# Performance work log

Hardware: AMD Instinct MI355X
Metric: run time of the kernel (lower is better)

Reference implementation:

```python
import jax, jax.numpy as jnp
import numpy as np


def setup_inputs() -> dict:
    key = jax.random.key(0)
    k1, k2 = jax.random.split(key)
    B, N, M, K = 8, 4096, 4096, 64
    input1 = jax.random.normal(k1, (B, N, K), dtype=jnp.float32)
    input2 = jax.random.normal(k2, (B, M, K), dtype=jnp.float32)
    return {"input1": input1, "input2": input2}


def reference(input1, input2):
    # Pairwise L2 distances via the ||x||^2 + ||y||^2 - 2<x,y> identity,
    # avoiding the O(B*N*M*K) broadcast-subtraction intermediate.
    x2 = jnp.sum(input1 * input1, axis=-1)                 # [B, N]
    y2 = jnp.sum(input2 * input2, axis=-1)                 # [B, M]
    xy = jnp.einsum('bnk,bmk->bnm', input1, input2)        # [B, N, M]
    sq = x2[:, :, None] + y2[:, None, :] - 2.0 * xy
    D = jnp.sqrt(jnp.maximum(sq, 0.0))                     # [B, N, M]
    dist0 = jnp.mean(jnp.min(D, axis=1), axis=1)           # min over N, mean over M
    dist1 = jnp.mean(jnp.min(D, axis=2), axis=1)           # min over M, mean over N
    loss = jnp.mean(dist0 + dist1)
    return loss
```

## Files before the change

### kernel.cpp

```cpp
#include <hip/hip_runtime.h>

#define BATCH 8
#define NPTS  4096
#define KD    64
#define MQ    4
#define WALK  8
#define FINF  3.0e38f

typedef float f32x4 __attribute__((ext_vector_type(4)));
typedef float f32x2 __attribute__((ext_vector_type(2)));
typedef short s16x8 __attribute__((ext_vector_type(8)));

__device__ __forceinline__ unsigned int f2bf(float f) {
  unsigned int u = __float_as_uint(f);
  u += 0x7FFFu + ((u >> 16) & 1u);
  return u >> 16;
}

__device__ __forceinline__ void stage16(const void* g, void* l) {
  __builtin_amdgcn_global_load_lds((const __attribute__((address_space(1))) void*)g,
                                   (__attribute__((address_space(3))) void*)l, 16, 0, 0);
}

__global__ __launch_bounds__(256)
void prep_kernel(const float* __restrict__ X, const float* __restrict__ Y,
                 unsigned int* __restrict__ Xbf, unsigned int* __restrict__ Ybf,
                 float* __restrict__ x2, float* __restrict__ y2,
                 unsigned int* __restrict__ counter) {
  int gid = blockIdx.x * 256 + threadIdx.x;
  if (gid == 0) *counter = 0;
  int row = gid >> 5;
  int ki  = gid & 31;
  bool isX = row < BATCH * NPTS;
  int r2 = row & (BATCH * NPTS - 1);
  const float* src = isX ? X : Y;
  f32x2 v = *(const f32x2*)(src + (size_t)r2 * KD + ki * 2);
  float s = v[0] * v[0] + v[1] * v[1];
  #pragma unroll
  for (int m = 16; m >= 1; m >>= 1) s += __shfl_xor(s, m, 64);
  unsigned int packed = (f2bf(v[1]) << 16) | f2bf(v[0]);
  (isX ? Xbf : Ybf)[r2 * 32 + ki] = packed;
  if (ki == 0) (isX ? x2 : y2)[r2] = s;
}

__global__ __launch_bounds__(256, 2)
void chamfer_main(const unsigned short* __restrict__ Xbf,
                  const unsigned short* __restrict__ Ybf,
                  const float* __restrict__ x2g, const float* __restrict__ y2g,
                  float* __restrict__ rowpart,
                  float* __restrict__ colpart) {
  __shared__ __align__(16) unsigned short Xs[128 * 64];
  __shared__ __align__(16) unsigned short Ys[2][128 * 64];
  __shared__ float l_cred[2 * 2 * 128];

  const int mq = blockIdx.x, ntile = blockIdx.y, b = blockIdx.z;
  const int n0 = ntile * 128;
  const int mbase = mq * (WALK * 128);
  const int t = threadIdx.x, w = t >> 6, lane = t & 63, c = lane & 15, q = lane >> 4;
  const int wr = (w >> 1) * 64, wc = (w & 1) * 64, rg = w >> 1;

  const int l8 = lane >> 3;
  const int lane_off = l8 * 128 + (((lane & 7) ^ l8) << 4);

  const char* Xg  = (const char*)(Xbf + (size_t)(b * NPTS + n0) * KD);
  const char* Yg0 = (const char*)(Ybf + (size_t)(b * NPTS + mbase) * KD);

  #pragma unroll
  for (int k = 0; k < 4; ++k) {
    int blockoff = (k * 32 + w * 8) * 128;
    int ldsoff   = (k * 256 + w * 64) * 16;
    stage16(Xg  + blockoff + lane_off, (char*)Xs    + ldsoff);
    stage16(Yg0 + blockoff + lane_off, (char*)Ys[0] + ldsoff);
  }

  const float* x2b = x2g + b * NPTS + n0;
  f32x4 x2r[4];
  #pragma unroll
  for (int i = 0; i < 4; ++i) x2r[i] = *(const f32x4*)(x2b + wr + i * 16 + q * 4);

  __syncthreads();

  const int cx = c & 7;
  s16x8 xf[4][2];
  #pragma unroll
  for (int i = 0; i < 4; ++i)
    #pragma unroll
    for (int ks = 0; ks < 2; ++ks)
      xf[i][ks] = *(const s16x8*)&Xs[(wr + i * 16 + c) * 64 + ((((ks << 2) + q) ^ cx) << 3)];

  float rm[4][4];
  #pragma unroll
  for (int i = 0; i < 4; ++i)
    #pragma unroll
    for (int r = 0; r < 4; ++r) rm[i][r] = FINF;

  const float* y2b = y2g + b * NPTS + mbase;
  float* colrow = colpart + (size_t)(ntile * 8 + b) * NPTS + mbase;
  const f32x4 zacc = {0.f, 0.f, 0.f, 0.f};

  #pragma unroll 2
  for (int tt = 0; tt < WALK; ++tt) {
    const unsigned short* cur = Ys[tt & 1];

    float y2c[4];
    #pragma unroll
    for (int j = 0; j < 4; ++j) y2c[j] = y2b[tt * 128 + wc + j * 16 + c];

    if (tt < WALK - 1) {
      const char* Ygt = Yg0 + (size_t)(tt + 1) * 128 * 128;
      unsigned short* nb = Ys[(tt + 1) & 1];
      #pragma unroll
      for (int k = 0; k < 4; ++k)
        stage16(Ygt + (k * 32 + w * 8) * 128 + lane_off,
                (char*)nb + (k * 256 + w * 64) * 16);
    }

    if (tt > 0 && t < 128) {
      int pt = tt - 1, pb = pt & 1;
      float v = fminf(l_cred[(pb * 2 + 0) * 128 + t], l_cred[(pb * 2 + 1) * 128 + t]);
      colrow[pt * 128 + t] = v + y2b[pt * 128 + t];
    }

    float cmj[4];
    #pragma unroll
    for (int j = 0; j < 4; ++j) {
      const unsigned short* yrow = &cur[(wc + j * 16 + c) * 64];
      s16x8 yf0 = *(const s16x8*)&yrow[(q ^ cx) << 3];
      s16x8 yf1 = *(const s16x8*)&yrow[((4 + q) ^ cx) << 3];
      f32x4 acc[4];
      #pragma unroll
      for (int i = 0; i < 4; ++i) {
        f32x4 a0 = __builtin_amdgcn_mfma_f32_16x16x32_bf16(xf[i][0], yf0, zacc, 0, 0, 0);
        acc[i] = __builtin_amdgcn_mfma_f32_16x16x32_bf16(xf[i][1], yf1, a0, 0, 0, 0);
      }
      float cm = FINF;
      #pragma unroll
      for (int i = 0; i < 4; ++i)
        #pragma unroll
        for (int r = 0; r < 4; ++r) {
          float v = acc[i][r];
          rm[i][r] = fminf(rm[i][r], fmaf(-2.f, v, y2c[j]));
          cm = fminf(cm, fmaf(-2.f, v, x2r[i][r]));
        }
      cm = fminf(cm, __shfl_xor(cm, 16, 64));
      cm = fminf(cm, __shfl_xor(cm, 32, 64));
      cmj[j] = cm;
    }
    float cmq = (q == 0) ? cmj[0] : (q == 1) ? cmj[1] : (q == 2) ? cmj[2] : cmj[3];
    l_cred[((tt & 1) * 2 + rg) * 128 + wc + q * 16 + c] = cmq;

    __syncthreads();
  }

  #pragma unroll
  for (int msk = 1; msk <= 8; msk <<= 1)
    #pragma unroll
    for (int i = 0; i < 4; ++i)
      #pragma unroll
      for (int r = 0; r < 4; ++r)
        rm[i][r] = fminf(rm[i][r], __shfl_xor(rm[i][r], msk, 64));
  float* l_redf = (float*)Xs;
  if (c == 0) {
    #pragma unroll
    for (int i = 0; i < 4; ++i) {
      f32x4 v = {rm[i][0], rm[i][1], rm[i][2], rm[i][3]};
      *(f32x4*)&l_redf[w * 64 + i * 16 + q * 4] = v;
    }
  }
  __syncthreads();

  if (t < 128) {
    {
      int pt = WALK - 1, pb = pt & 1;
      float v = fminf(l_cred[(pb * 2 + 0) * 128 + t], l_cred[(pb * 2 + 1) * 128 + t]);
      colrow[pt * 128 + t] = v + y2b[pt * 128 + t];
    }
    int g = t >> 6, lr = t & 63;
    float v = fminf(l_redf[(g * 2) * 64 + lr], l_redf[(g * 2 + 1) * 64 + lr]);
    rowpart[mq * (BATCH * NPTS) + b * NPTS + n0 + t] = v + x2b[t];
  }
}

__global__ __launch_bounds__(256)
void reduce_kernel(const float* __restrict__ rowpart, const float* __restrict__ colpart,
                   float* __restrict__ partials, unsigned int* __restrict__ counter,
                   float* __restrict__ out) {
  int i = blockIdx.x * 256 + threadIdx.x;
  const int TOT = BATCH * NPTS;
  float rv = FINF;
  #pragma unroll
  for (int s = 0; s < MQ; ++s) rv = fminf(rv, rowpart[s * TOT + i]);
  float s0 = sqrtf(fmaxf(rv, 0.f));
  float cv = FINF;
  #pragma unroll
  for (int nt = 0; nt < 32; ++nt) cv = fminf(cv, colpart[nt * TOT + i]);
  s0 += sqrtf(fmaxf(cv, 0.f));
  #pragma unroll
  for (int m = 32; m >= 1; m >>= 1) s0 += __shfl_xor(s0, m, 64);
  __shared__ float wsum[4];
  if ((threadIdx.x & 63) == 0) wsum[threadIdx.x >> 6] = s0;
  __syncthreads();

  if (threadIdx.x < 64) {
    unsigned int ticket = 0;
    if (threadIdx.x == 0) {
      float bsum = wsum[0] + wsum[1] + wsum[2] + wsum[3];
      atomicExch(&partials[blockIdx.x], bsum);
      __threadfence();
      ticket = atomicAdd(counter, 1);
    }
    ticket = __shfl(ticket, 0, 64);
    if (ticket == 127) {
      float v = atomicAdd(&partials[threadIdx.x], 0.0f) +
                atomicAdd(&partials[threadIdx.x + 64], 0.0f);
      #pragma unroll
      for (int m = 32; m >= 1; m >>= 1) v += __shfl_xor(v, m, 64);
      if (threadIdx.x == 0) out[0] = v * (1.0f / (float)TOT);
    }
  }
}

extern "C" void kernel_launch(void* const* d_in, const int* in_sizes, int n_in,
                              void* d_out, int out_size, void* d_ws, size_t ws_size,
                              hipStream_t stream) {
  const float* X = (const float*)d_in[0];
  const float* Y = (const float*)d_in[1];
  float* out = (float*)d_out;

  char* ws = (char*)d_ws;
  unsigned int* Xbf = (unsigned int*)ws;
  unsigned int* Ybf = (unsigned int*)(ws + (4u << 20));
  float* x2 = (float*)(ws + (8u << 20));
  float* y2 = (float*)(ws + (8u << 20) + (128u << 10));
  float* rowpart = (float*)(ws + (8u << 20) + (256u << 10));
  float* colpart = (float*)(ws + (9u << 20) + (256u << 10));
  float* partials = (float*)(ws + (13u << 20) + (256u << 10));
  unsigned int* counter = (unsigned int*)(partials + 128);

  prep_kernel<<<dim3(2 * BATCH * NPTS * 32 / 256), dim3(256), 0, stream>>>(
      X, Y, Xbf, Ybf, x2, y2, counter);

  chamfer_main<<<dim3(MQ, 32, 8), dim3(256), 0, stream>>>(
      (const unsigned short*)Xbf, (const unsigned short*)Ybf, x2, y2, rowpart, colpart);

  reduce_kernel<<<dim3(BATCH * NPTS / 256), dim3(256), 0, stream>>>(
      rowpart, colpart, partials, counter, out);
}
```

Before: 106.8 us.

## Load X fragments directly from global and cut one cross-lane shuffle per column

Removes the shared-memory staging buffer for the X tile. Each wave now loads its bf16 X fragments straight from global memory into registers, which frees LDS (possibly improving occupancy) and drops one LDS round trip. The column-min reduction now does a single xor-16 shuffle instead of two and writes four partial slots per column into a padded LDS buffer, with the final min over the four slots done by the reducing threads. The trade-off is uncoalesced 16-byte global loads for X and extra LDS reads in the column reduction.

```diff
diff --git a/kernel.cpp b/kernel.cpp
--- a/kernel.cpp
+++ b/kernel.cpp
@@ -49,9 +49,9 @@
                   const float* __restrict__ x2g, const float* __restrict__ y2g,
                   float* __restrict__ rowpart,
                   float* __restrict__ colpart) {
-  __shared__ __align__(16) unsigned short Xs[128 * 64];
   __shared__ __align__(16) unsigned short Ys[2][128 * 64];
-  __shared__ float l_cred[2 * 2 * 128];
+  __shared__ float l_credq[2 * 4 * 132];
+  __shared__ float l_redf[256];
 
   const int mq = blockIdx.x, ntile = blockIdx.y, b = blockIdx.z;
   const int n0 = ntile * 128;
@@ -62,16 +62,20 @@
   const int l8 = lane >> 3;
   const int lane_off = l8 * 128 + (((lane & 7) ^ l8) << 4);
 
-  const char* Xg  = (const char*)(Xbf + (size_t)(b * NPTS + n0) * KD);
+  const unsigned short* Xrow = Xbf + (size_t)(b * NPTS + n0) * KD;
   const char* Yg0 = (const char*)(Ybf + (size_t)(b * NPTS + mbase) * KD);
 
   #pragma unroll
-  for (int k = 0; k < 4; ++k) {
-    int blockoff = (k * 32 + w * 8) * 128;
-    int ldsoff   = (k * 256 + w * 64) * 16;
-    stage16(Xg  + blockoff + lane_off, (char*)Xs    + ldsoff);
-    stage16(Yg0 + blockoff + lane_off, (char*)Ys[0] + ldsoff);
-  }
+  for (int k = 0; k < 4; ++k)
+    stage16(Yg0 + (k * 32 + w * 8) * 128 + lane_off,
+            (char*)Ys[0] + (k * 256 + w * 64) * 16);
+
+  s16x8 xf[4][2];
+  #pragma unroll
+  for (int i = 0; i < 4; ++i)
+    #pragma unroll
+    for (int ks = 0; ks < 2; ++ks)
+      xf[i][ks] = *(const s16x8*)&Xrow[(size_t)(wr + i * 16 + c) * KD + (ks * 4 + q) * 8];
 
   const float* x2b = x2g + b * NPTS + n0;
   f32x4 x2r[4];
@@ -80,20 +84,13 @@
 
   __syncthreads();
 
+  float rm[4][4];
+  #pragma unroll
+  for (int i = 0; i < 4; ++i)
+    #pragma unroll
+    for (int r = 0; r < 4; ++r) rm[i][r] = FINF;
+
   const int cx = c & 7;
-  s16x8 xf[4][2];
-  #pragma unroll
-  for (int i = 0; i < 4; ++i)
-    #pragma unroll
-    for (int ks = 0; ks < 2; ++ks)
-      xf[i][ks] = *(const s16x8*)&Xs[(wr + i * 16 + c) * 64 + ((((ks << 2) + q) ^ cx) << 3)];
-
-  float rm[4][4];
-  #pragma unroll
-  for (int i = 0; i < 4; ++i)
-    #pragma unroll
-    for (int r = 0; r < 4; ++r) rm[i][r] = FINF;
-
   const float* y2b = y2g + b * NPTS + mbase;
   float* colrow = colpart + (size_t)(ntile * 8 + b) * NPTS + mbase;
   const f32x4 zacc = {0.f, 0.f, 0.f, 0.f};
@@ -117,7 +114,8 @@
 
     if (tt > 0 && t < 128) {
       int pt = tt - 1, pb = pt & 1;
-      float v = fminf(l_cred[(pb * 2 + 0) * 128 + t], l_cred[(pb * 2 + 1) * 128 + t]);
+      float v = fminf(fminf(l_credq[(pb * 4 + 0) * 132 + t], l_credq[(pb * 4 + 1) * 132 + t]),
+                      fminf(l_credq[(pb * 4 + 2) * 132 + t], l_credq[(pb * 4 + 3) * 132 + t]));
       colrow[pt * 128 + t] = v + y2b[pt * 128 + t];
     }
 
@@ -143,11 +141,17 @@
           cm = fminf(cm, fmaf(-2.f, v, x2r[i][r]));
         }
       cm = fminf(cm, __shfl_xor(cm, 16, 64));
-      cm = fminf(cm, __shfl_xor(cm, 32, 64));
       cmj[j] = cm;
     }
-    float cmq = (q == 0) ? cmj[0] : (q == 1) ? cmj[1] : (q == 2) ? cmj[2] : cmj[3];
-    l_cred[((tt & 1) * 2 + rg) * 128 + wc + q * 16 + c] = cmq;
+    {
+      int s = rg * 2 + (q >> 1);
+      int jA = (q & 1) * 2;
+      float sA = (q & 1) ? cmj[2] : cmj[0];
+      float sB = (q & 1) ? cmj[3] : cmj[1];
+      float* dst = &l_credq[((tt & 1) * 4 + s) * 132 + wc + c];
+      dst[jA * 16]      = sA;
+      dst[jA * 16 + 16] = sB;
+    }
 
     __syncthreads();
   }
@@ -159,7 +163,6 @@
       #pragma unroll
       for (int r = 0; r < 4; ++r)
         rm[i][r] = fminf(rm[i][r], __shfl_xor(rm[i][r], msk, 64));
-  float* l_redf = (float*)Xs;
   if (c == 0) {
     #pragma unroll
     for (int i = 0; i < 4; ++i) {
@@ -172,7 +175,8 @@
   if (t < 128) {
     {
       int pt = WALK - 1, pb = pt & 1;
-      float v = fminf(l_cred[(pb * 2 + 0) * 128 + t], l_cred[(pb * 2 + 1) * 128 + t]);
+      float v = fminf(fminf(l_credq[(pb * 4 + 0) * 132 + t], l_credq[(pb * 4 + 1) * 132 + t]),
+                      fminf(l_credq[(pb * 4 + 2) * 132 + t], l_credq[(pb * 4 + 3) * 132 + t]));
       colrow[pt * 128 + t] = v + y2b[pt * 128 + t];
     }
     int g = t >> 6, lr = t & 63;
```

Result: faster. 104.0 us (median of 2 runs) (-2.6%).
